# Kernel optimization log

Hardware: AMD Instinct MI355X
Metric: run time of the kernel (lower is better)

## Reference

```python
import jax, jax.numpy as jnp
import numpy as np

N_LEVELS = 16
N_FEATS = 2
LOG2_T = 19
TABLE_SIZE = 1 << LOG2_T
BASE_RES = 16
FINEST_RES = 512
DIM = 3
N_POINTS = 2_000_000
PRIMES = jnp.array([1, 2654435761, 805459861], dtype=jnp.uint32)


def _hash_encode(x01, tables, resolutions):
    """Multi-resolution hash grid encoding with trilinear interpolation.
    x01: [N, D] in [0, 1]; tables: [L, T, F]; resolutions: [L] float.
    Returns [N, L*F]."""
    N, D = x01.shape
    T = tables.shape[1]
    # all 2^D corner offsets of the enclosing voxel, shape [2^D, D]
    offsets = jnp.array([[(i >> d) & 1 for d in range(D)] for i in range(1 << D)],
                        dtype=jnp.float32)

    def per_level(table, res):
        pos = x01 * res                      # [N, D]
        p0 = jnp.floor(pos)
        w = pos - p0                         # fractional part, [N, D]
        corners = p0[None, :, :] + offsets[:, None, :]      # [2^D, N, D]
        ci = corners.astype(jnp.uint32)
        hp = ci * PRIMES[None, None, :D]                    # uint32 wraps mod 2^32
        h = hp[..., 0]
        for d in range(1, D):
            h = h ^ hp[..., d]
        idx = (h & jnp.uint32(T - 1)).astype(jnp.int32)     # [2^D, N]
        feats = table[idx]                                  # gather, [2^D, N, F]
        # trilinear weights: prod_d (w_d if corner bit set else 1-w_d)
        wc = jnp.prod(jnp.where(offsets[:, None, :] > 0, w[None], 1.0 - w[None]),
                      axis=-1)                              # [2^D, N]
        return jnp.sum(wc[..., None] * feats, axis=0)       # [N, F]

    f = jax.vmap(per_level)(tables, resolutions)            # [L, N, F]
    return jnp.transpose(f, (1, 0, 2)).reshape(N, -1)       # [N, L*F]


def setup_inputs() -> dict:
    key = jax.random.key(0)
    ks = jax.random.split(key, 8)
    x = jax.random.uniform(ks[0], (N_POINTS, DIM), jnp.float32, -1.0, 1.0)
    tables = jax.random.uniform(ks[1], (N_LEVELS, TABLE_SIZE, N_FEATS),
                                jnp.float32, -1e-4, 1e-4)
    b = np.exp((np.log(FINEST_RES) - np.log(BASE_RES)) / (N_LEVELS - 1))
    resolutions = jnp.asarray(np.floor(BASE_RES * b ** np.arange(N_LEVELS)),
                              dtype=jnp.float32)
    in_dim = N_LEVELS * N_FEATS  # 32
    W1 = jax.random.normal(ks[2], (in_dim, 64), jnp.float32) * (1.0 / np.sqrt(in_dim))
    b1 = jnp.zeros((64,), jnp.float32)
    W2 = jax.random.normal(ks[3], (64, 64), jnp.float32) * (1.0 / 8.0)
    b2 = jnp.zeros((64,), jnp.float32)
    W3 = jax.random.normal(ks[4], (64, 1), jnp.float32) * (1.0 / 8.0)
    b3 = jnp.zeros((1,), jnp.float32)
    return {"x": x, "tables": tables, "resolutions": resolutions,
            "W1": W1, "b1": b1, "W2": W2, "b2": b2, "W3": W3, "b3": b3}


def reference(x, tables, resolutions, W1, b1, W2, b2, W3, b3):
    x01 = x / 2.0 + 0.5                       # map [-1,1] -> [0,1]
    a = _hash_encode(x01, tables, resolutions)  # [N, 32]
    h = jax.nn.relu(a @ W1 + b1)
    h = jax.nn.relu(h @ W2 + b2)
    return h @ W3 + b3                        # [N, 1]
```

## Files before the change

### kernel.cpp

```cpp
#include <hip/hip_runtime.h>
#include <hip/hip_bf16.h>
#include <stdint.h>

#define N_LEVELS   16
#define LOG2_T     19
#define TABLE_SIZE (1u << LOG2_T)
#define PRIME_Y    2654435761u
#define PRIME_Z    805459861u

#define NB        32768
#define SORT_B    256
#define SORT_T    512
#define CVT_B     2048

typedef float v4f __attribute__((ext_vector_type(4)));
typedef _Float16 v8h __attribute__((ext_vector_type(8)));

__device__ __forceinline__ uint32_t part1by2(uint32_t v) {
    v &= 0x3FFu;
    v = (v | (v << 16)) & 0x030000FFu;
    v = (v | (v <<  8)) & 0x0300F00Fu;
    v = (v | (v <<  4)) & 0x030C30C3u;
    v = (v | (v <<  2)) & 0x09249249u;
    return v;
}
__device__ __forceinline__ uint32_t morton_key(float xr, float yr, float zr) {
    int vx = (int)((xr * 0.5f + 0.5f) * 32.0f);
    int vy = (int)((yr * 0.5f + 0.5f) * 32.0f);
    int vz = (int)((zr * 0.5f + 0.5f) * 32.0f);
    vx = vx < 0 ? 0 : (vx > 31 ? 31 : vx);
    vy = vy < 0 ? 0 : (vy > 31 ? 31 : vy);
    vz = vz < 0 ? 0 : (vz > 31 ? 31 : vz);
    return part1by2((uint32_t)vx) | (part1by2((uint32_t)vy) << 1)
         | (part1by2((uint32_t)vz) << 2);
}

__global__ __launch_bounds__(SORT_T)
void hist_cvt_kernel(const float* __restrict__ x, uint32_t* __restrict__ g_hist,
                     int n, int chunk,
                     const float* __restrict__ tables,
                     uint32_t* __restrict__ tab16)
{
    __shared__ uint32_t pack[NB / 2];
    if (blockIdx.x >= SORT_B) {
        const int cb = blockIdx.x - SORT_B;
        const size_t base_pair = (size_t)cb * SORT_T * 4;
        #pragma unroll
        for (int k = 0; k < 4; ++k) {
            const size_t e2 = base_pair + (size_t)k * SORT_T + threadIdx.x;
            const size_t base = e2 * 2;
            const float4 v = *(const float4*)(tables + base * 2);
            union { _Float16 h[2]; uint32_t u; } p0, p1;
            p0.h[0] = (_Float16)v.x; p0.h[1] = (_Float16)v.y;
            p1.h[0] = (_Float16)v.z; p1.h[1] = (_Float16)v.w;
            *(uint2*)(tab16 + base) = make_uint2(p0.u, p1.u);
        }
        return;
    }
    const int b = blockIdx.x, t = threadIdx.x;
    for (int w = t; w < NB / 2; w += SORT_T) pack[w] = 0;
    __syncthreads();
    const int beg = b * chunk;
    const int end = (beg + chunk < n) ? (beg + chunk) : n;
    for (int i = beg + t; i < end; i += SORT_T) {
        const uint32_t key = morton_key(x[3*i], x[3*i+1], x[3*i+2]);
        atomicAdd(&pack[key >> 1], 1u << ((key & 1u) << 4));
    }
    __syncthreads();
    uint32_t* __restrict__ dst = g_hist + (size_t)b * NB;
    for (int w = t; w < NB / 2; w += SORT_T) {
        const uint32_t p = pack[w];
        dst[2*w]     = p & 0xFFFFu;
        dst[2*w + 1] = p >> 16;
    }
}

__global__ __launch_bounds__(256)
void scan_cols_kernel(const uint32_t* __restrict__ g_hist,
                      uint32_t* __restrict__ g_part,
                      uint32_t* __restrict__ totals)
{
    const int key = blockIdx.x * 256 + threadIdx.x;
    uint32_t run = 0;
    #pragma unroll 8
    for (int b = 0; b < SORT_B; ++b) {
        const size_t idx = (size_t)b * NB + key;
        const uint32_t v = g_hist[idx];
        g_part[idx] = run;
        run += v;
    }
    totals[key] = run;
}

__global__ void scan_block_kernel(const uint32_t* __restrict__ counts,
                                  uint32_t* __restrict__ prefix,
                                  uint32_t* __restrict__ blocksum) {
    __shared__ uint32_t s[256];
    const int t = threadIdx.x;
    const int i = blockIdx.x * 256 + t;
    const uint32_t v = counts[i];
    s[t] = v; __syncthreads();
    #pragma unroll
    for (int d = 1; d < 256; d <<= 1) {
        const uint32_t u = (t >= d) ? s[t - d] : 0;
        __syncthreads();
        s[t] += u;
        __syncthreads();
    }
    prefix[i] = s[t] - v;
    if (t == 255) blocksum[blockIdx.x] = s[255];
}

__global__ void scan_top_kernel(const uint32_t* __restrict__ blocksum,
                                uint32_t* __restrict__ blockbase, int nb) {
    __shared__ uint32_t s[1024];
    const int t = threadIdx.x;
    const uint32_t v = (t < nb) ? blocksum[t] : 0;
    s[t] = v; __syncthreads();
    #pragma unroll
    for (int d = 1; d < 1024; d <<= 1) {
        const uint32_t u = (t >= d) ? s[t - d] : 0;
        __syncthreads();
        s[t] += u;
        __syncthreads();
    }
    if (t < nb) blockbase[t] = s[t] - v;
}

__global__ __launch_bounds__(SORT_T)
void scatter_kernel(const float* __restrict__ x,
                    const uint32_t* __restrict__ pref,
                    const uint32_t* __restrict__ bbase,
                    const uint32_t* __restrict__ g_part,
                    float4* __restrict__ xs4,
                    int* __restrict__ perm,
                    int n, int chunk)
{
    __shared__ uint32_t pack[NB / 2];
    const int b = blockIdx.x, t = threadIdx.x;
    for (int w = t; w < NB / 2; w += SORT_T) pack[w] = 0;
    __syncthreads();
    const uint32_t* __restrict__ part = g_part + (size_t)b * NB;
    const int beg = b * chunk;
    const int end = (beg + chunk < n) ? (beg + chunk) : n;
    for (int i = beg + t; i < end; i += SORT_T) {
        const float a = x[3*i], c = x[3*i+1], d = x[3*i+2];
        const uint32_t key = morton_key(a, c, d);
        const uint32_t sh = (key & 1u) << 4;
        uint32_t r = atomicAdd(&pack[key >> 1], 1u << sh);
        r = (r >> sh) & 0xFFFFu;
        const uint32_t pos = pref[key] + bbase[key >> 8] + part[key] + r;
        xs4[pos]  = make_float4(a, c, d, 0.0f);
        perm[pos] = i;
    }
}

__device__ __forceinline__ float2 unpk16(uint32_t u) {
    union { uint32_t u; _Float16 h[2]; } c; c.u = u;
    return make_float2((float)c.h[0], (float)c.h[1]);
}

__global__ __launch_bounds__(256)
void encode_f16_kernel(const float4* __restrict__ xs4,
                       const uint32_t* __restrict__ tab16,
                       const float* __restrict__ resolutions,
                       uint32_t* __restrict__ a_ws2,
                       int n, int half)
{
    const int l = blockIdx.y;
    int p0 = blockIdx.x * blockDim.x + threadIdx.x;
    if (p0 >= half) p0 = half - 1;
    int p1 = p0 + half;
    if (p1 >= n) p1 = n - 1;

    const float res = resolutions[l];
    const uint32_t* __restrict__ tab = tab16 + (size_t)l * (size_t)TABLE_SIZE;
    const int pp[2] = { p0, p1 };

    uint2    wreg[2][4];
    uint32_t swp[2];
    float    wxa[2], wya[2], wza[2];

    #pragma unroll
    for (int s = 0; s < 2; ++s) {
        const float4 xv = xs4[pp[s]];
        const float x0 = xv.x * 0.5f + 0.5f;
        const float x1 = xv.y * 0.5f + 0.5f;
        const float x2 = xv.z * 0.5f + 0.5f;

        const float px = x0 * res, py = x1 * res, pz = x2 * res;
        const float fx = floorf(px), fy = floorf(py), fz = floorf(pz);
        wxa[s] = px - fx; wya[s] = py - fy; wza[s] = pz - fz;
        const uint32_t cx = (uint32_t)fx;
        const uint32_t cy = (uint32_t)fy;
        const uint32_t cz = (uint32_t)fz;

        const uint32_t hy0 = cy * PRIME_Y, hy1 = hy0 + PRIME_Y;
        const uint32_t hz0 = cz * PRIME_Z, hz1 = hz0 + PRIME_Z;
        const uint32_t hyz[4] = { hy0 ^ hz0, hy1 ^ hz0, hy0 ^ hz1, hy1 ^ hz1 };

        uint32_t sm = 0;
        if ((cx & 1u) == 0u) {
            #pragma unroll
            for (int q = 0; q < 4; ++q) {
                const uint32_t idx_a = (cx ^ hyz[q]) & (TABLE_SIZE - 1u);
                wreg[s][q] = *(const uint2*)(tab + (idx_a & ~1u));
                sm |= (idx_a & 1u) << q;
            }
        } else {
            #pragma unroll
            for (int q = 0; q < 4; ++q) {
                const uint32_t idx_a = (cx        ^ hyz[q]) & (TABLE_SIZE - 1u);
                const uint32_t idx_b = ((cx + 1u) ^ hyz[q]) & (TABLE_SIZE - 1u);
                wreg[s][q].x = tab[idx_a];
                wreg[s][q].y = tab[idx_b];
            }
        }
        swp[s] = sm;
    }

    #pragma unroll
    for (int s = 0; s < 2; ++s) {
        const float wx = wxa[s], wy = wya[s], wz = wza[s];
        const float wx0 = 1.0f - wx, wy0 = 1.0f - wy, wz0 = 1.0f - wz;
        float f0 = 0.0f, f1 = 0.0f;
        #pragma unroll
        for (int q = 0; q < 4; ++q) {
            const bool sw = (swp[s] >> q) & 1u;
            const uint32_t wa = sw ? wreg[s][q].y : wreg[s][q].x;
            const uint32_t wb = sw ? wreg[s][q].x : wreg[s][q].y;
            const float2 ca = unpk16(wa);
            const float2 cb = unpk16(wb);
            const float yf = (q & 1) ? wy : wy0;
            const float zf = (q & 2) ? wz : wz0;
            const float wgt_a = (wx0 * yf) * zf;
            const float wgt_b = (wx  * yf) * zf;
            f0 = fmaf(wgt_a, ca.x, f0);
            f1 = fmaf(wgt_a, ca.y, f1);
            f0 = fmaf(wgt_b, cb.x, f0);
            f1 = fmaf(wgt_b, cb.y, f1);
        }
        union { _Float16 h[2]; uint32_t u; } pk;
        pk.h[0] = (_Float16)(f0 * 256.0f);
        pk.h[1] = (_Float16)(f1 * 256.0f);
        __builtin_nontemporal_store(pk.u, a_ws2 + (size_t)l * n + pp[s]);
    }
}

__global__ __launch_bounds__(256, 8)
void encode_kernel(const float4* __restrict__ xs4,
                   const float* __restrict__ tables,
                   const float* __restrict__ resolutions,
                   uint32_t* __restrict__ a_ws2,
                   int n)
{
    const int l = blockIdx.y;
    int p = blockIdx.x * blockDim.x + threadIdx.x;
    if (p >= n) p = n - 1;

    const float4 xv = xs4[p];
    const float x0 = xv.x * 0.5f + 0.5f;
    const float x1 = xv.y * 0.5f + 0.5f;
    const float x2 = xv.z * 0.5f + 0.5f;

    const float res = resolutions[l];
    const float px = x0 * res, py = x1 * res, pz = x2 * res;
    const float fx = floorf(px), fy = floorf(py), fz = floorf(pz);
    const float wx = px - fx, wy = py - fy, wz = pz - fz;
    const uint32_t cx = (uint32_t)fx;
    const uint32_t cy = (uint32_t)fy;
    const uint32_t cz = (uint32_t)fz;

    const uint32_t hy0 = cy * PRIME_Y, hy1 = hy0 + PRIME_Y;
    const uint32_t hz0 = cz * PRIME_Z, hz1 = hz0 + PRIME_Z;

    const float wx0 = 1.0f - wx, wy0 = 1.0f - wy, wz0 = 1.0f - wz;

    const float* __restrict__ tab = tables + (size_t)l * (size_t)TABLE_SIZE * 2u;

    const uint32_t hyz[4] = { hy0 ^ hz0, hy1 ^ hz0, hy0 ^ hz1, hy1 ^ hz1 };

    float2 cva[4], cvb[4];

    if ((cx & 1u) == 0u) {
        #pragma unroll
        for (int q = 0; q < 4; ++q) {
            const uint32_t idx_a = (cx ^ hyz[q]) & (TABLE_SIZE - 1u);
            const uint32_t base  = idx_a & ~1u;
            const float4 f4 = *(const float4*)(tab + 2u * base);
            const bool hi = (idx_a & 1u) != 0u;
            cva[q] = hi ? make_float2(f4.z, f4.w) : make_float2(f4.x, f4.y);
            cvb[q] = hi ? make_float2(f4.x, f4.y) : make_float2(f4.z, f4.w);
        }
    } else {
        const uint32_t hx0 = cx, hx1 = cx + 1u;
        #pragma unroll
        for (int q = 0; q < 4; ++q) {
            const uint32_t idx_a = (hx0 ^ hyz[q]) & (TABLE_SIZE - 1u);
            const uint32_t idx_b = (hx1 ^ hyz[q]) & (TABLE_SIZE - 1u);
            cva[q] = *(const float2*)(tab + 2u * idx_a);
            cvb[q] = *(const float2*)(tab + 2u * idx_b);
        }
    }

    float f0 = 0.0f, f1 = 0.0f;
    #pragma unroll
    for (int q = 0; q < 4; ++q) {
        const float yf = (q & 1) ? wy : wy0;
        const float zf = (q & 2) ? wz : wz0;
        const float wgt_a = (wx0 * yf) * zf;
        const float wgt_b = (wx  * yf) * zf;
        f0 = fmaf(wgt_a, cva[q].x, f0);
        f1 = fmaf(wgt_a, cva[q].y, f1);
        f0 = fmaf(wgt_b, cvb[q].x, f0);
        f1 = fmaf(wgt_b, cvb[q].y, f1);
    }

    union { _Float16 h[2]; uint32_t u; } pk;
    pk.h[0] = (_Float16)(f0 * 256.0f);
    pk.h[1] = (_Float16)(f1 * 256.0f);
    __builtin_nontemporal_store(pk.u, a_ws2 + (size_t)l * n + p);
}

#define MLP_CB1 4096
#define MLP_CB2 4160
#define MLP_CW3 4224
__global__ __launch_bounds__(256, 2)
void mlp_mfma_kernel(const uint32_t* __restrict__ a_ws2,
                     const float* __restrict__ W1,
                     const float* __restrict__ b1,
                     const float* __restrict__ W2,
                     const float* __restrict__ b2,
                     const float* __restrict__ W3,
                     const float* __restrict__ b3,
                     const int* __restrict__ perm,
                     float* __restrict__ out,
                     int n)
{
    __shared__ float lds[4 * 64 * 16 + 192];

    const int lane    = threadIdx.x & 63;
    const int wave_id = threadIdx.x >> 6;
    const int m       = lane & 15;
    const int q       = lane >> 4;
    float* __restrict__ myl = &lds[wave_id * 1024];

    if (threadIdx.x < 64) {
        lds[MLP_CB1 + threadIdx.x] = 256.0f * b1[threadIdx.x];
        lds[MLP_CB2 + threadIdx.x] = 256.0f * b2[threadIdx.x];
        lds[MLP_CW3 + threadIdx.x] = W3[threadIdx.x];
    }

    const float b3s = b3[0];

    v8h a1[4];
    #pragma unroll
    for (int t = 0; t < 4; ++t)
        #pragma unroll
        for (int j = 0; j < 8; ++j)
            a1[t][j] = (_Float16)W1[(8 * q + j) * 64 + 16 * t + m];

    v8h a2[2][4];
    #pragma unroll
    for (int c = 0; c < 2; ++c)
        #pragma unroll
        for (int t = 0; t < 4; ++t)
            #pragma unroll
            for (int j = 0; j < 8; ++j)
                a2[c][t][j] = (_Float16)W2[(32 * c + 8 * q + j) * 64 + 16 * t + m];

    __syncthreads();

    const int nt = (n + 15) >> 4;
    const int stride = gridDim.x * 4;
    const int gw = blockIdx.x * 4 + wave_id;
    if (gw >= nt) return;

    union BF { uint32_t w[4]; v8h h; };

    v8h bh;
    {
        const int p0 = gw * 16;
        const int pr = (p0 + m < n) ? (p0 + m) : (n - 1);
        BF ub;
        #pragma unroll
        for (int lv = 0; lv < 4; ++lv)
            ub.w[lv] = __builtin_nontemporal_load(
                a_ws2 + (size_t)(4 * q + lv) * n + pr);
        bh = ub.h;
    }

    for (int tile = gw; tile < nt; tile += stride) {
        const int p0 = tile * 16;

        v8h bhn = bh;
        const int nx = tile + stride;
        if (nx < nt) {
            const int p0n = nx * 16;
            const int prn = (p0n + m < n) ? (p0n + m) : (n - 1);
            BF ub;
            #pragma unroll
            for (int lv = 0; lv < 4; ++lv)
                ub.w[lv] = __builtin_nontemporal_load(
                    a_ws2 + (size_t)(4 * q + lv) * n + prn);
            bhn = ub.h;
        }

        v4f acc1[4];
        #pragma unroll
        for (int t = 0; t < 4; ++t) {
            acc1[t] = *(const v4f*)&lds[MLP_CB1 + 16 * t + 4 * q];
            acc1[t] = __builtin_amdgcn_mfma_f32_16x16x32_f16(a1[t], bh, acc1[t], 0, 0, 0);
        }

        #pragma unroll
        for (int t = 0; t < 4; ++t)
            #pragma unroll
            for (int r = 0; r < 4; ++r)
                myl[(16 * t + 4 * q + r) * 16 + m] = fmaxf(acc1[t][r], 0.0f);
        __threadfence_block();

        v8h b2h[2];
        #pragma unroll
        for (int c = 0; c < 2; ++c)
            #pragma unroll
            for (int j = 0; j < 8; ++j)
                b2h[c][j] = (_Float16)myl[(32 * c + 8 * q + j) * 16 + m];

        v4f acc2[4];
        #pragma unroll
        for (int t = 0; t < 4; ++t) {
            acc2[t] = *(const v4f*)&lds[MLP_CB2 + 16 * t + 4 * q];
            acc2[t] = __builtin_amdgcn_mfma_f32_16x16x32_f16(a2[0][t], b2h[0], acc2[t], 0, 0, 0);
            acc2[t] = __builtin_amdgcn_mfma_f32_16x16x32_f16(a2[1][t], b2h[1], acc2[t], 0, 0, 0);
        }

        float partial = 0.0f;
        #pragma unroll
        for (int t = 0; t < 4; ++t) {
            const v4f w3q = *(const v4f*)&lds[MLP_CW3 + 16 * t + 4 * q];
            #pragma unroll
            for (int r = 0; r < 4; ++r)
                partial = fmaf(fmaxf(acc2[t][r], 0.0f), w3q[r], partial);
        }

        partial += __shfl_xor(partial, 16);
        partial += __shfl_xor(partial, 32);

        if (q == 0 && p0 + m < n)
            out[perm[p0 + m]] = partial * (1.0f / 256.0f) + b3s;

        bh = bhn;
    }
}

__global__ __launch_bounds__(256, 4)
void hashgrid_mlp_fused(const float* __restrict__ x,
                        const float* __restrict__ tables,
                        const float* __restrict__ resolutions,
                        const float* __restrict__ W1,
                        const float* __restrict__ b1,
                        const float* __restrict__ W2,
                        const float* __restrict__ b2,
                        const float* __restrict__ W3,
                        const float* __restrict__ b3,
                        float* __restrict__ out,
                        int n)
{
    const int i  = blockIdx.x * blockDim.x + threadIdx.x;
    const int ip = (i < n) ? i : (n - 1);

    const float x0 = x[3 * ip + 0] * 0.5f + 0.5f;
    const float x1 = x[3 * ip + 1] * 0.5f + 0.5f;
    const float x2 = x[3 * ip + 2] * 0.5f + 0.5f;

    float h1[64];
    #pragma unroll
    for (int j = 0; j < 64; ++j) h1[j] = b1[j];

    #pragma unroll
    for (int l = 0; l < N_LEVELS; ++l) {
        const float res = resolutions[l];
        const float px = x0 * res, py = x1 * res, pz = x2 * res;
        const float fx = floorf(px), fy = floorf(py), fz = floorf(pz);
        const float wx = px - fx, wy = py - fy, wz = pz - fz;
        const uint32_t cx = (uint32_t)fx;
        const uint32_t cy = (uint32_t)fy;
        const uint32_t cz = (uint32_t)fz;
        const uint32_t hx0 = cx,           hx1 = cx + 1u;
        const uint32_t hy0 = cy * PRIME_Y, hy1 = hy0 + PRIME_Y;
        const uint32_t hz0 = cz * PRIME_Z, hz1 = hz0 + PRIME_Z;
        const float wx0 = 1.0f - wx, wy0 = 1.0f - wy, wz0 = 1.0f - wz;
        const float* __restrict__ tab = tables + (size_t)l * (size_t)TABLE_SIZE * 2u;

        float f0 = 0.0f, f1 = 0.0f;
        #pragma unroll
        for (int c = 0; c < 8; ++c) {
            const uint32_t h = ((c & 1) ? hx1 : hx0) ^
                               ((c & 2) ? hy1 : hy0) ^
                               ((c & 4) ? hz1 : hz0);
            const uint32_t idx = h & (TABLE_SIZE - 1u);
            const float2 fv = *(const float2*)(tab + 2u * idx);
            const float wgt = ((c & 1) ? wx : wx0) *
                              ((c & 2) ? wy : wy0) *
                              ((c & 4) ? wz : wz0);
            f0 = fmaf(wgt, fv.x, f0);
            f1 = fmaf(wgt, fv.y, f1);
        }
        const float* __restrict__ w1a = W1 + (2 * l + 0) * 64;
        const float* __restrict__ w1b = W1 + (2 * l + 1) * 64;
        #pragma unroll
        for (int j = 0; j < 64; ++j)
            h1[j] = fmaf(f1, w1b[j], fmaf(f0, w1a[j], h1[j]));
    }

    #pragma unroll
    for (int j = 0; j < 64; ++j) h1[j] = fmaxf(h1[j], 0.0f);

    float accum = b3[0];
    #pragma unroll
    for (int half = 0; half < 2; ++half) {
        float h2[32];
        #pragma unroll
        for (int j = 0; j < 32; ++j) h2[j] = b2[half * 32 + j];
        #pragma unroll
        for (int k = 0; k < 64; ++k) {
            const float hk = h1[k];
            const float* __restrict__ w2row = W2 + k * 64 + half * 32;
            #pragma unroll
            for (int j = 0; j < 32; ++j)
                h2[j] = fmaf(hk, w2row[j], h2[j]);
        }
        #pragma unroll
        for (int j = 0; j < 32; ++j)
            accum = fmaf(fmaxf(h2[j], 0.0f), W3[half * 32 + j], accum);
    }
    out[ip] = accum;
}

extern "C" void kernel_launch(void* const* d_in, const int* in_sizes, int n_in,
                              void* d_out, int out_size, void* d_ws, size_t ws_size,
                              hipStream_t stream) {
    const float* x           = (const float*)d_in[0];
    const float* tables      = (const float*)d_in[1];
    const float* resolutions = (const float*)d_in[2];
    const float* W1          = (const float*)d_in[3];
    const float* b1          = (const float*)d_in[4];
    const float* W2          = (const float*)d_in[5];
    const float* b2          = (const float*)d_in[6];
    const float* W3          = (const float*)d_in[7];
    const float* b3          = (const float*)d_in[8];
    float* out               = (float*)d_out;

    const int n = out_size;
    const int block = 256;
    const int grid_pts = (n + block - 1) / block;
    const int chunk = (n + SORT_B - 1) / SORT_B;
    const int half = (n + 1) / 2;
    const int grid_half = (half + block - 1) / block;

    size_t off = 0;
    #define CARVE(bytes) (off = (off + 255) & ~(size_t)255, off += (bytes), off - (bytes))
    const size_t aws_off   = CARVE((size_t)16 * n * sizeof(uint32_t));
    const size_t xs_off    = CARVE((size_t)n * sizeof(float4));
    const size_t perm_off  = CARVE((size_t)n * sizeof(int));
    const size_t tot_off   = CARVE((size_t)NB * sizeof(uint32_t));
    const size_t pref_off  = CARVE((size_t)NB * sizeof(uint32_t));
    const size_t bsum_off  = CARVE(1024 * sizeof(uint32_t));
    const size_t bbase_off = CARVE(1024 * sizeof(uint32_t));
    const size_t total_ws_B = off;
    const size_t tab16_off = CARVE((size_t)N_LEVELS * TABLE_SIZE * sizeof(uint32_t));
    const size_t total_ws_A = off;
    #undef CARVE

    if (ws_size >= total_ws_B) {
        const bool f16tab = (ws_size >= total_ws_A);
        char* ws = (char*)d_ws;
        uint32_t* a_ws2  = (uint32_t*)(ws + aws_off);
        uint32_t* g_hist = (uint32_t*)(ws + aws_off);
        uint32_t* g_part = (uint32_t*)(ws + aws_off + (size_t)SORT_B * NB * 4);
        float4*   xs4    = (float4*)(ws + xs_off);
        int*      perm   = (int*)(ws + perm_off);
        uint32_t* totals = (uint32_t*)(ws + tot_off);
        uint32_t* pref   = (uint32_t*)(ws + pref_off);
        uint32_t* bsum   = (uint32_t*)(ws + bsum_off);
        uint32_t* bbase  = (uint32_t*)(ws + bbase_off);
        uint32_t* tab16  = (uint32_t*)(ws + tab16_off);

        const int hist_grid = SORT_B + (f16tab ? CVT_B : 0);
        hist_cvt_kernel<<<hist_grid, SORT_T, 0, stream>>>(
            x, g_hist, n, chunk, tables, f16tab ? tab16 : (uint32_t*)nullptr);
        scan_cols_kernel<<<NB / 256, block, 0, stream>>>(g_hist, g_part, totals);
        scan_block_kernel<<<NB / 256, block, 0, stream>>>(totals, pref, bsum);
        scan_top_kernel<<<1, 1024, 0, stream>>>(bsum, bbase, NB / 256);
        scatter_kernel<<<SORT_B, SORT_T, 0, stream>>>(
            x, pref, bbase, g_part, xs4, perm, n, chunk);

        if (f16tab) {
            dim3 grid_enc(grid_half, N_LEVELS);
            encode_f16_kernel<<<grid_enc, block, 0, stream>>>(
                xs4, tab16, resolutions, a_ws2, n, half);
        } else {
            dim3 grid_enc(grid_pts, N_LEVELS);
            encode_kernel<<<grid_enc, block, 0, stream>>>(
                xs4, tables, resolutions, a_ws2, n);
        }
        mlp_mfma_kernel<<<1024, block, 0, stream>>>(a_ws2, W1, b1, W2, b2, W3, b3,
                                                    perm, out, n);
    } else {
        hashgrid_mlp_fused<<<grid_pts, block, 0, stream>>>(
            x, tables, resolutions, W1, b1, W2, b2, W3, b3, out, n);
    }
}
```

Before: 575.2 us.

## Merge two-level scan into one kernel and replace scatter-write with gather unscatter

Replaces the block scan and top scan kernels with a single 1024-thread kernel that scans all 32K bucket counts, dropping one launch and one level of indirection in the scatter. The MLP kernel now writes outputs contiguously in sorted order, and a new unscatter kernel gathers them back to the original order through an inverse-rank array written by the scatter. This turns the random scattered output stores plus the perm loads into coalesced writes, at the cost of an extra launch, an extra buffer and a random gather read.

```diff
diff --git a/kernel.cpp b/kernel.cpp
--- a/kernel.cpp
+++ b/kernel.cpp
@@ -92,31 +92,17 @@
     totals[key] = run;
 }
 
-__global__ void scan_block_kernel(const uint32_t* __restrict__ counts,
-                                  uint32_t* __restrict__ prefix,
-                                  uint32_t* __restrict__ blocksum) {
-    __shared__ uint32_t s[256];
-    const int t = threadIdx.x;
-    const int i = blockIdx.x * 256 + t;
-    const uint32_t v = counts[i];
-    s[t] = v; __syncthreads();
-    #pragma unroll
-    for (int d = 1; d < 256; d <<= 1) {
-        const uint32_t u = (t >= d) ? s[t - d] : 0;
-        __syncthreads();
-        s[t] += u;
-        __syncthreads();
-    }
-    prefix[i] = s[t] - v;
-    if (t == 255) blocksum[blockIdx.x] = s[255];
-}
-
-__global__ void scan_top_kernel(const uint32_t* __restrict__ blocksum,
-                                uint32_t* __restrict__ blockbase, int nb) {
+__global__ __launch_bounds__(1024)
+void scan32k_kernel(const uint32_t* __restrict__ cnt,
+                    uint32_t* __restrict__ base)
+{
     __shared__ uint32_t s[1024];
     const int t = threadIdx.x;
-    const uint32_t v = (t < nb) ? blocksum[t] : 0;
-    s[t] = v; __syncthreads();
+    uint32_t loc[32];
+    uint32_t sum = 0;
+    #pragma unroll
+    for (int j = 0; j < 32; ++j) { loc[j] = cnt[t * 32 + j]; sum += loc[j]; }
+    s[t] = sum; __syncthreads();
     #pragma unroll
     for (int d = 1; d < 1024; d <<= 1) {
         const uint32_t u = (t >= d) ? s[t - d] : 0;
@@ -124,16 +110,17 @@
         s[t] += u;
         __syncthreads();
     }
-    if (t < nb) blockbase[t] = s[t] - v;
+    uint32_t run = s[t] - sum;
+    #pragma unroll
+    for (int j = 0; j < 32; ++j) { base[t * 32 + j] = run; run += loc[j]; }
 }
 
 __global__ __launch_bounds__(SORT_T)
 void scatter_kernel(const float* __restrict__ x,
-                    const uint32_t* __restrict__ pref,
-                    const uint32_t* __restrict__ bbase,
+                    const uint32_t* __restrict__ base,
                     const uint32_t* __restrict__ g_part,
                     float4* __restrict__ xs4,
-                    int* __restrict__ perm,
+                    int* __restrict__ rank_inv,
                     int n, int chunk)
 {
     __shared__ uint32_t pack[NB / 2];
@@ -149,9 +136,9 @@
         const uint32_t sh = (key & 1u) << 4;
         uint32_t r = atomicAdd(&pack[key >> 1], 1u << sh);
         r = (r >> sh) & 0xFFFFu;
-        const uint32_t pos = pref[key] + bbase[key >> 8] + part[key] + r;
-        xs4[pos]  = make_float4(a, c, d, 0.0f);
-        perm[pos] = i;
+        const uint32_t pos = base[key] + part[key] + r;
+        xs4[pos]    = make_float4(a, c, d, 0.0f);
+        rank_inv[i] = (int)pos;
     }
 }
 
@@ -333,8 +320,7 @@
                      const float* __restrict__ b2,
                      const float* __restrict__ W3,
                      const float* __restrict__ b3,
-                     const int* __restrict__ perm,
-                     float* __restrict__ out,
+                     float* __restrict__ outs,
                      int n)
 {
     __shared__ float lds[4 * 64 * 16 + 192];
@@ -448,10 +434,18 @@
         partial += __shfl_xor(partial, 32);
 
         if (q == 0 && p0 + m < n)
-            out[perm[p0 + m]] = partial * (1.0f / 256.0f) + b3s;
+            outs[p0 + m] = partial * (1.0f / 256.0f) + b3s;
 
         bh = bhn;
     }
+}
+
+__global__ __launch_bounds__(256)
+void unscatter_kernel(const float* __restrict__ outs,
+                      const int* __restrict__ rank_inv,
+                      float* __restrict__ out, int n) {
+    const int i = blockIdx.x * blockDim.x + threadIdx.x;
+    if (i < n) out[i] = outs[rank_inv[i]];
 }
 
 __global__ __launch_bounds__(256, 4)
@@ -563,11 +557,10 @@
     #define CARVE(bytes) (off = (off + 255) & ~(size_t)255, off += (bytes), off - (bytes))
     const size_t aws_off   = CARVE((size_t)16 * n * sizeof(uint32_t));
     const size_t xs_off    = CARVE((size_t)n * sizeof(float4));
-    const size_t perm_off  = CARVE((size_t)n * sizeof(int));
+    const size_t rank_off  = CARVE((size_t)n * sizeof(int));
+    const size_t outs_off  = CARVE((size_t)n * sizeof(float));
     const size_t tot_off   = CARVE((size_t)NB * sizeof(uint32_t));
-    const size_t pref_off  = CARVE((size_t)NB * sizeof(uint32_t));
-    const size_t bsum_off  = CARVE(1024 * sizeof(uint32_t));
-    const size_t bbase_off = CARVE(1024 * sizeof(uint32_t));
+    const size_t base_off  = CARVE((size_t)NB * sizeof(uint32_t));
     const size_t total_ws_B = off;
     const size_t tab16_off = CARVE((size_t)N_LEVELS * TABLE_SIZE * sizeof(uint32_t));
     const size_t total_ws_A = off;
@@ -580,21 +573,19 @@
         uint32_t* g_hist = (uint32_t*)(ws + aws_off);
         uint32_t* g_part = (uint32_t*)(ws + aws_off + (size_t)SORT_B * NB * 4);
         float4*   xs4    = (float4*)(ws + xs_off);
-        int*      perm   = (int*)(ws + perm_off);
+        int*      rank   = (int*)(ws + rank_off);
+        float*    outs   = (float*)(ws + outs_off);
         uint32_t* totals = (uint32_t*)(ws + tot_off);
-        uint32_t* pref   = (uint32_t*)(ws + pref_off);
-        uint32_t* bsum   = (uint32_t*)(ws + bsum_off);
-        uint32_t* bbase  = (uint32_t*)(ws + bbase_off);
+        uint32_t* base   = (uint32_t*)(ws + base_off);
         uint32_t* tab16  = (uint32_t*)(ws + tab16_off);
 
         const int hist_grid = SORT_B + (f16tab ? CVT_B : 0);
         hist_cvt_kernel<<<hist_grid, SORT_T, 0, stream>>>(
             x, g_hist, n, chunk, tables, f16tab ? tab16 : (uint32_t*)nullptr);
         scan_cols_kernel<<<NB / 256, block, 0, stream>>>(g_hist, g_part, totals);
-        scan_block_kernel<<<NB / 256, block, 0, stream>>>(totals, pref, bsum);
-        scan_top_kernel<<<1, 1024, 0, stream>>>(bsum, bbase, NB / 256);
+        scan32k_kernel<<<1, 1024, 0, stream>>>(totals, base);
         scatter_kernel<<<SORT_B, SORT_T, 0, stream>>>(
-            x, pref, bbase, g_part, xs4, perm, n, chunk);
+            x, base, g_part, xs4, rank, n, chunk);
 
         if (f16tab) {
             dim3 grid_enc(grid_half, N_LEVELS);
@@ -606,7 +597,8 @@
                 xs4, tables, resolutions, a_ws2, n);
         }
         mlp_mfma_kernel<<<1024, block, 0, stream>>>(a_ws2, W1, b1, W2, b2, W3, b3,
-                                                    perm, out, n);
+                                                    outs, n);
+        unscatter_kernel<<<grid_pts, block, 0, stream>>>(outs, rank, out, n);
     } else {
         hashgrid_mlp_fused<<<grid_pts, block, 0, stream>>>(
             x, tables, resolutions, W1, b1, W2, b2, W3, b3, out, n);
```

Measured after the change: 550.1 us. -4.4%, faster.
